# Kernel optimization log

Measured on AMD Instinct MI355X. Metric: run time of the kernel, lower is better.

The kernel has to match this reference:

```python
import jax, jax.numpy as jnp
import numpy as np

N = 50000        # nodes
E = 800000       # edges (avg degree 16)
IN = 256         # in_size
H = 4            # heads
C = 32           # out_size per head
NEG_SLOPE = 0.2  # PyG GATConv leaky_relu slope
LN_EPS = 1e-5


def setup_inputs() -> dict:
    key = jax.random.key(0)
    ks = jax.random.split(key, 6)
    x = jax.random.normal(ks[0], (N, IN), dtype=jnp.float32)
    edge_index = jax.random.randint(ks[1], (2, E), 0, N, dtype=jnp.int32)
    W = jax.random.normal(ks[2], (IN, H * C), dtype=jnp.float32) * 0.05
    att_src = jax.random.normal(ks[3], (H, C), dtype=jnp.float32) * 0.05
    att_dst = jax.random.normal(ks[4], (H, C), dtype=jnp.float32) * 0.05
    bias = jnp.zeros((H * C,), dtype=jnp.float32)
    ln_gamma = jnp.ones((H * C,), dtype=jnp.float32)
    ln_beta = jnp.zeros((H * C,), dtype=jnp.float32)
    return {"x": x, "edge_index": edge_index, "W": W, "att_src": att_src,
            "att_dst": att_dst, "bias": bias, "ln_gamma": ln_gamma,
            "ln_beta": ln_beta}


def _segment_softmax(alpha, seg, num_segments):
    # alpha: [E, H], softmax over edges sharing the same destination node.
    amax = jax.ops.segment_max(alpha, seg, num_segments=num_segments)  # [N, H]
    amax = jnp.where(jnp.isfinite(amax), amax, 0.0)  # nodes with no in-edges
    ex = jnp.exp(alpha - amax[seg])
    denom = jax.ops.segment_sum(ex, seg, num_segments=num_segments)    # [N, H]
    return ex / (denom[seg] + 1e-16)


def reference(x, edge_index, W, att_src, att_dst, bias, ln_gamma, ln_beta):
    # --- GATConv (concat=True) ---
    x_lin = (x @ W).reshape(N, H, C)                    # [N, H, C]
    a_src = jnp.sum(x_lin * att_src, axis=-1)           # [N, H]
    a_dst = jnp.sum(x_lin * att_dst, axis=-1)           # [N, H]
    src, dst = edge_index[0], edge_index[1]             # messages src -> dst
    alpha = a_src[src] + a_dst[dst]                     # [E, H]
    alpha = jnp.where(alpha >= 0, alpha, NEG_SLOPE * alpha)
    alpha = _segment_softmax(alpha, dst, N)             # [E, H]
    msg = x_lin[src] * alpha[..., None]                 # [E, H, C]
    out = jax.ops.segment_sum(msg, dst, num_segments=N) # [N, H, C]
    out = out.reshape(N, H * C) + bias                  # [N, H*C]
    # --- LayerNorm over feature dim ---
    mu = jnp.mean(out, axis=-1, keepdims=True)
    var = jnp.mean(jnp.square(out - mu), axis=-1, keepdims=True)
    out = (out - mu) * jax.lax.rsqrt(var + LN_EPS) * ln_gamma + ln_beta
    # --- activation ---
    return jax.nn.relu(out)
```

## Files before the change

### kernel.cpp

```cpp
#include <hip/hip_runtime.h>

#define NNODES 50000
#define NEDGES 800000
#define INFEAT 256
#define HC 128
#define NH 4
#define CPH 32
#define LSTRIDE 264
#define WSTR 68

typedef unsigned int uint32;
typedef unsigned short u16;
typedef short short8 __attribute__((ext_vector_type(8)));
typedef float f32x4 __attribute__((ext_vector_type(4)));

__device__ __forceinline__ float b2f(u16 s) {
    uint32 u = ((uint32)s) << 16;
    return __builtin_bit_cast(float, u);
}
__device__ __forceinline__ u16 f2bf(float x) {
    uint32 u = __builtin_bit_cast(uint32, x);
    uint32 r = (u + 0x7FFFu + ((u >> 16) & 1u)) >> 16;
    return (u16)r;
}
__device__ __forceinline__ bool probe_bf16(const void* gamma) {
    return ((const uint32*)gamma)[0] == 0x3F803F80u;
}
__device__ __forceinline__ float expleaky(float a) {
    return __expf(fmaxf(a, 0.2f * a));
}

__global__ __launch_bounds__(256) void wtp_kernel(const void* __restrict__ W,
                                                  const void* __restrict__ gm,
                                                  u16* __restrict__ wtp,
                                                  int* __restrict__ count) {
    const bool isbf = probe_bf16(gm);
    int c = blockIdx.x * 256 + threadIdx.x;
    int kt = c >> 9, nt = (c >> 6) & 7, l = c & 63;
    int r = l & 15, quad = l >> 4;
    int n = nt * 16 + r;
    int kbase = kt * 32 + quad * 8;
    u16 vals[8];
#pragma unroll
    for (int j = 0; j < 8; ++j) {
        int k = kbase + j;
        vals[j] = isbf ? ((const u16*)W)[k * HC + n] : f2bf(((const float*)W)[k * HC + n]);
    }
    *(uint4*)(wtp + (size_t)c * 8) = *(const uint4*)vals;
    uint4 z = {0u, 0u, 0u, 0u};
    uint4* cz = (uint4*)count;
    for (int i = c; i < NNODES / 4; i += 4096) cz[i] = z;
}

__global__ __launch_bounds__(256) void hist_kernel(const int* __restrict__ ei,
                                                   int* __restrict__ count,
                                                   int* __restrict__ rank) {
    int eb = blockIdx.x * 1024 + threadIdx.x;
#pragma unroll
    for (int rep = 0; rep < 4; ++rep) {
        int e = eb + rep * 256;
        if (e < NEDGES) rank[e] = atomicAdd(&count[ei[NEDGES + e]], 1);
    }
}

__global__ __launch_bounds__(256) void gemm_mfma(const void* __restrict__ x,
                                                 const uint4* __restrict__ wtp,
                                                 const void* __restrict__ att_src,
                                                 const void* __restrict__ att_dst,
                                                 const void* __restrict__ gm,
                                                 u16* __restrict__ xlin,
                                                 float* __restrict__ asrc,
                                                 float* __restrict__ adst) {
    __shared__ u16 atile[4 * 16 * LSTRIDE];
    const bool isbf = probe_bf16(gm);
    const int tid = threadIdx.x;
    const int wv = tid >> 6;
    const int lane = tid & 63;
    int wave = blockIdx.x * 4 + wv;
    int r = lane & 15;
    int quad = lane >> 4;
    int m0 = wave * 16;
    u16* my = atile + wv * (16 * LSTRIDE);

    if (isbf) {
#pragma unroll
        for (int rep = 0; rep < 8; ++rep) {
            int idx = rep * 64 + lane;
            int row = idx >> 5;
            int ch  = idx & 31;
            int gr = m0 + row;
            if (gr > NNODES - 1) gr = NNODES - 1;
            uint4 q = *(const uint4*)((const u16*)x + (size_t)gr * INFEAT + ch * 8);
            *(uint4*)(my + row * LSTRIDE + ch * 8) = q;
        }
    } else {
#pragma unroll
        for (int rep = 0; rep < 16; ++rep) {
            int idx = rep * 64 + lane;
            int row = idx >> 6;
            int c4  = idx & 63;
            int gr = m0 + row;
            if (gr > NNODES - 1) gr = NNODES - 1;
            float4 f = *(const float4*)((const float*)x + (size_t)gr * INFEAT + c4 * 4);
            u16 v[4] = {f2bf(f.x), f2bf(f.y), f2bf(f.z), f2bf(f.w)};
            *(uint2*)(my + row * LSTRIDE + c4 * 4) = *(const uint2*)v;
        }
    }

    f32x4 acc[8];
#pragma unroll
    for (int nt = 0; nt < 8; ++nt) acc[nt] = (f32x4){0.f, 0.f, 0.f, 0.f};

#pragma unroll
    for (int kt = 0; kt < 8; ++kt) {
        short8 afrag = __builtin_bit_cast(short8,
            *(const uint4*)(my + r * LSTRIDE + kt * 32 + quad * 8));
#pragma unroll
        for (int nt = 0; nt < 8; ++nt) {
            short8 bfrag = __builtin_bit_cast(short8, wtp[(kt * 8 + nt) * 64 + lane]);
            acc[nt] = __builtin_amdgcn_mfma_f32_16x16x32_bf16(afrag, bfrag, acc[nt], 0, 0, 0);
        }
    }
#pragma unroll
    for (int nt = 0; nt < 8; ++nt) {
#pragma unroll
        for (int reg = 0; reg < 4; ++reg) {
            int grow = m0 + quad * 4 + reg;
            if (grow < NNODES) xlin[(size_t)grow * HC + nt * 16 + r] = f2bf(acc[nt][reg]);
        }
    }

    float asv[8], adv[8];
#pragma unroll
    for (int nt = 0; nt < 8; ++nt) {
        int c = nt * 16 + r;
        if (isbf) {
            asv[nt] = b2f(((const u16*)att_src)[c]);
            adv[nt] = b2f(((const u16*)att_dst)[c]);
        } else {
            asv[nt] = ((const float*)att_src)[c];
            adv[nt] = ((const float*)att_dst)[c];
        }
    }
    float psrc[4][4], pdst[4][4];
#pragma unroll
    for (int h = 0; h < 4; ++h)
#pragma unroll
        for (int reg = 0; reg < 4; ++reg) { psrc[h][reg] = 0.f; pdst[h][reg] = 0.f; }
#pragma unroll
    for (int nt = 0; nt < 8; ++nt) {
        const int h = nt >> 1;
#pragma unroll
        for (int reg = 0; reg < 4; ++reg) {
            psrc[h][reg] = fmaf(acc[nt][reg], asv[nt], psrc[h][reg]);
            pdst[h][reg] = fmaf(acc[nt][reg], adv[nt], pdst[h][reg]);
        }
    }
#pragma unroll
    for (int m = 1; m < 16; m <<= 1) {
#pragma unroll
        for (int h = 0; h < 4; ++h)
#pragma unroll
            for (int reg = 0; reg < 4; ++reg) {
                psrc[h][reg] += __shfl_xor(psrc[h][reg], m);
                pdst[h][reg] += __shfl_xor(pdst[h][reg], m);
            }
    }
#pragma unroll
    for (int reg = 0; reg < 4; ++reg)
#pragma unroll
        for (int h = 0; h < 4; ++h)
            if (r == reg * 4 + h) {
                int grow = m0 + quad * 4 + reg;
                if (grow < NNODES) {
                    asrc[grow * 4 + h] = psrc[h][reg];
                    adst[grow * 4 + h] = pdst[h][reg];
                }
            }
}

__global__ __launch_bounds__(256) void blkred_kernel(const int* __restrict__ count,
                                                     int* __restrict__ blksum) {
    int i = blockIdx.x * 256 + threadIdx.x;
    int v = (i < NNODES) ? count[i] : 0;
#pragma unroll
    for (int m = 1; m < 64; m <<= 1) v += __shfl_xor(v, m);
    __shared__ int s[4];
    if ((threadIdx.x & 63) == 0) s[threadIdx.x >> 6] = v;
    __syncthreads();
    if (threadIdx.x == 0) blksum[blockIdx.x] = s[0] + s[1] + s[2] + s[3];
}

__global__ __launch_bounds__(256) void scanout_kernel(const int* __restrict__ count,
                                                      const int* __restrict__ blksum,
                                                      int* __restrict__ offsets) {
    __shared__ int sb[256];
    __shared__ int sd[256];
    const int nblk = (NNODES + 255) / 256;
    int t = threadIdx.x;
    int bv = (t < nblk) ? blksum[t] : 0;
    sb[t] = bv;
    __syncthreads();
    for (int off = 1; off < 256; off <<= 1) {
        int tv = (t >= off) ? sb[t - off] : 0;
        __syncthreads();
        sb[t] += tv;
        __syncthreads();
    }
    int base = sb[blockIdx.x] - blksum[blockIdx.x];

    int i = blockIdx.x * 256 + t;
    int v = (i < NNODES) ? count[i] : 0;
    sd[t] = v;
    __syncthreads();
    for (int off = 1; off < 256; off <<= 1) {
        int tv = (t >= off) ? sd[t - off] : 0;
        __syncthreads();
        sd[t] += tv;
        __syncthreads();
    }
    if (i < NNODES) offsets[i] = base + sd[t] - v;
    if (i == 0) offsets[NNODES] = NEDGES;
}

__global__ __launch_bounds__(256) void scatter_kernel(const int* __restrict__ ei,
                                                      const int* __restrict__ offsets,
                                                      const int* __restrict__ rank,
                                                      int* __restrict__ col) {
    int e = blockIdx.x * 256 + threadIdx.x;
    if (e >= NEDGES) return;
    int d = ei[NEDGES + e];
    col[offsets[d] + rank[e]] = ei[e];
}

__global__ __launch_bounds__(256) void node_kernel(const u16* __restrict__ xlin,
                                                   const float* __restrict__ asrc,
                                                   const float* __restrict__ adst,
                                                   const int* __restrict__ offsets,
                                                   const int* __restrict__ col,
                                                   const void* __restrict__ bias,
                                                   const void* __restrict__ gamma,
                                                   const void* __restrict__ beta,
                                                   void* __restrict__ out) {
    __shared__ float wlds[4][4 * WSTR];
    __shared__ int   slds[4][64];
    const bool isbf = probe_bf16(gamma);
    const int wv = threadIdx.x >> 6;
    const int lane = threadIdx.x & 63;
    int node = blockIdx.x * 4 + wv;
    int h = lane >> 4;
    int f2 = lane * 2;
    int start = offsets[node];
    int end = offsets[node + 1];
    float4 ad4 = *(const float4*)(adst + (size_t)node * 4);

    float dsum = 0.f, acc0 = 0.f, acc1 = 0.f;
    float* wmy = wlds[wv];
    int* smy = slds[wv];

    for (int base = start; base < end; base += 64) {
        int cnt = end - base;
        if (cnt > 64) cnt = 64;
        float4 w4 = {0.f, 0.f, 0.f, 0.f};
        int src = 0;
        if (lane < cnt) {
            src = col[base + lane];
            float4 as4 = *(const float4*)(asrc + (size_t)src * 4);
            w4.x = expleaky(as4.x + ad4.x);
            w4.y = expleaky(as4.y + ad4.y);
            w4.z = expleaky(as4.z + ad4.z);
            w4.w = expleaky(as4.w + ad4.w);
        }
        smy[lane] = src;
        wmy[0 * WSTR + lane] = w4.x;
        wmy[1 * WSTR + lane] = w4.y;
        wmy[2 * WSTR + lane] = w4.z;
        wmy[3 * WSTR + lane] = w4.w;

        const float* wh = wmy + h * WSTR;
        int j = 0;
        for (; j + 7 < cnt; j += 8) {
            float4 wa = *(const float4*)(wh + j);
            float4 wb = *(const float4*)(wh + j + 4);
            int4 sa = *(const int4*)(smy + j);
            int4 sb = *(const int4*)(smy + j + 4);
            uint32 pf[8];
            pf[0] = *(const uint32*)(xlin + (size_t)sa.x * HC + f2);
            pf[1] = *(const uint32*)(xlin + (size_t)sa.y * HC + f2);
            pf[2] = *(const uint32*)(xlin + (size_t)sa.z * HC + f2);
            pf[3] = *(const uint32*)(xlin + (size_t)sa.w * HC + f2);
            pf[4] = *(const uint32*)(xlin + (size_t)sb.x * HC + f2);
            pf[5] = *(const uint32*)(xlin + (size_t)sb.y * HC + f2);
            pf[6] = *(const uint32*)(xlin + (size_t)sb.z * HC + f2);
            pf[7] = *(const uint32*)(xlin + (size_t)sb.w * HC + f2);
            float wv8[8] = {wa.x, wa.y, wa.z, wa.w, wb.x, wb.y, wb.z, wb.w};
#pragma unroll
            for (int k = 0; k < 8; ++k) {
                float w = wv8[k];
                dsum += w;
                float x0 = __builtin_bit_cast(float, pf[k] << 16);
                float x1 = __builtin_bit_cast(float, pf[k] & 0xffff0000u);
                acc0 = fmaf(x0, w, acc0);
                acc1 = fmaf(x1, w, acc1);
            }
        }
        for (; j + 3 < cnt; j += 4) {
            float4 wa = *(const float4*)(wh + j);
            int4 sa = *(const int4*)(smy + j);
            uint32 pf[4];
            pf[0] = *(const uint32*)(xlin + (size_t)sa.x * HC + f2);
            pf[1] = *(const uint32*)(xlin + (size_t)sa.y * HC + f2);
            pf[2] = *(const uint32*)(xlin + (size_t)sa.z * HC + f2);
            pf[3] = *(const uint32*)(xlin + (size_t)sa.w * HC + f2);
            float wv4[4] = {wa.x, wa.y, wa.z, wa.w};
#pragma unroll
            for (int k = 0; k < 4; ++k) {
                float w = wv4[k];
                dsum += w;
                float x0 = __builtin_bit_cast(float, pf[k] << 16);
                float x1 = __builtin_bit_cast(float, pf[k] & 0xffff0000u);
                acc0 = fmaf(x0, w, acc0);
                acc1 = fmaf(x1, w, acc1);
            }
        }
        for (; j < cnt; ++j) {
            float w = wh[j];
            int c = smy[j];
            uint32 p = *(const uint32*)(xlin + (size_t)c * HC + f2);
            dsum += w;
            float x0 = __builtin_bit_cast(float, p << 16);
            float x1 = __builtin_bit_cast(float, p & 0xffff0000u);
            acc0 = fmaf(x0, w, acc0);
            acc1 = fmaf(x1, w, acc1);
        }
    }
    float rden = 1.f / (dsum + 1e-16f);

    float bi0, bi1, g0, g1, be0, be1;
    if (isbf) {
        uint32 bb = ((const uint32*)bias)[lane];
        uint32 gg = ((const uint32*)gamma)[lane];
        uint32 eb = ((const uint32*)beta)[lane];
        bi0 = b2f((u16)(bb & 0xffffu)); bi1 = b2f((u16)(bb >> 16));
        g0  = b2f((u16)(gg & 0xffffu)); g1  = b2f((u16)(gg >> 16));
        be0 = b2f((u16)(eb & 0xffffu)); be1 = b2f((u16)(eb >> 16));
    } else {
        float2 tb = ((const float2*)bias)[lane];
        float2 tg = ((const float2*)gamma)[lane];
        float2 te = ((const float2*)beta)[lane];
        bi0 = tb.x; bi1 = tb.y; g0 = tg.x; g1 = tg.y; be0 = te.x; be1 = te.y;
    }
    float v0 = fmaf(acc0, rden, bi0);
    float v1 = fmaf(acc1, rden, bi1);
    float s2 = v0 + v1;
    float q2 = v0 * v0 + v1 * v1;
#pragma unroll
    for (int m = 1; m < 64; m <<= 1) {
        s2 += __shfl_xor(s2, m);
        q2 += __shfl_xor(q2, m);
    }
    float mean = s2 * (1.f / 128.f);
    float var = q2 * (1.f / 128.f) - mean * mean;
    float inv = rsqrtf(var + 1e-5f);
    float d0 = v0 - mean, d1 = v1 - mean;
    float o0 = fmaxf(fmaf(d0 * inv, g0, be0), 0.f);
    float o1 = fmaxf(fmaf(d1 * inv, g1, be1), 0.f);
    if (isbf) {
        uint32 po = (uint32)f2bf(o0) | ((uint32)f2bf(o1) << 16);
        ((uint32*)out)[(size_t)node * 64 + lane] = po;
    } else {
        float2 po; po.x = o0; po.y = o1;
        ((float2*)out)[(size_t)node * 64 + lane] = po;
    }
}

extern "C" void kernel_launch(void* const* d_in, const int* in_sizes, int n_in,
                              void* d_out, int out_size, void* d_ws, size_t ws_size,
                              hipStream_t stream) {
    const void* x       = d_in[0];
    const int*  ei      = (const int*)d_in[1];
    const void* W       = d_in[2];
    const void* att_src = d_in[3];
    const void* att_dst = d_in[4];
    const void* bias    = d_in[5];
    const void* gamma   = d_in[6];
    const void* beta    = d_in[7];

    char* w = (char*)d_ws;
    size_t off = 0;
    u16* xlin    = (u16*)(w + off);   off += 12800000;
    u16* wtp     = (u16*)(w + off);   off += 65536;
    float* asrc  = (float*)(w + off); off += 800000;
    float* adst  = (float*)(w + off); off += 800000;
    int* count   = (int*)(w + off);   off += 200000;
    int* offsets = (int*)(w + off);   off += 200016;
    int* rank    = (int*)(w + off);   off += 3200000;
    int* blksum  = (int*)(w + off);   off += 1024;
    int* col     = (int*)(w + off);   off += 3200000;

    const int NBLK = (NNODES + 255) / 256;
    wtp_kernel<<<16, 256, 0, stream>>>(W, gamma, wtp, count);
    hist_kernel<<<(NEDGES + 1023) / 1024, 256, 0, stream>>>(ei, count, rank);
    gemm_mfma<<<(NNODES + 63) / 64, 256, 0, stream>>>(x, (const uint4*)wtp, att_src, att_dst,
                                                      gamma, xlin, asrc, adst);
    blkred_kernel<<<NBLK, 256, 0, stream>>>(count, blksum);
    scanout_kernel<<<NBLK, 256, 0, stream>>>(count, blksum, offsets);
    scatter_kernel<<<(NEDGES + 255) / 256, 256, 0, stream>>>(ei, offsets, rank, col);
    node_kernel<<<NNODES / 4, 256, 0, stream>>>(xlin, asrc, adst, offsets, col,
                                                bias, gamma, beta, d_out);
}
```

Baseline: 212.7 us.

## Replace global atomic degree histogram with per-block LDS histograms plus column prefix

Degree counting no longer does one global atomicAdd per edge. The edges are split across 64 blocks, and each block builds a packed 16-bit histogram in a 100KB shared-memory array and writes it to global memory. A new colsum kernel turns these per-block histograms into per-block base offsets and total counts, and the scatter kernel adds the base for the edge's block when placing it. This removes contended global atomics but launches only 64 blocks and adds about 19MB of extra global traffic plus a random base lookup per edge in scatter.

```diff
diff --git a/kernel.cpp b/kernel.cpp
--- a/kernel.cpp
+++ b/kernel.cpp
@@ -8,6 +8,8 @@
 #define CPH 32
 #define LSTRIDE 264
 #define WSTR 68
+#define NB 64
+#define EPB (NEDGES / NB)
 
 typedef unsigned int uint32;
 typedef unsigned short u16;
@@ -32,8 +34,7 @@
 
 __global__ __launch_bounds__(256) void wtp_kernel(const void* __restrict__ W,
                                                   const void* __restrict__ gm,
-                                                  u16* __restrict__ wtp,
-                                                  int* __restrict__ count) {
+                                                  u16* __restrict__ wtp) {
     const bool isbf = probe_bf16(gm);
     int c = blockIdx.x * 256 + threadIdx.x;
     int kt = c >> 9, nt = (c >> 6) & 7, l = c & 63;
@@ -47,20 +48,41 @@
         vals[j] = isbf ? ((const u16*)W)[k * HC + n] : f2bf(((const float*)W)[k * HC + n]);
     }
     *(uint4*)(wtp + (size_t)c * 8) = *(const uint4*)vals;
-    uint4 z = {0u, 0u, 0u, 0u};
-    uint4* cz = (uint4*)count;
-    for (int i = c; i < NNODES / 4; i += 4096) cz[i] = z;
-}
-
-__global__ __launch_bounds__(256) void hist_kernel(const int* __restrict__ ei,
-                                                   int* __restrict__ count,
-                                                   int* __restrict__ rank) {
-    int eb = blockIdx.x * 1024 + threadIdx.x;
-#pragma unroll
-    for (int rep = 0; rep < 4; ++rep) {
-        int e = eb + rep * 256;
-        if (e < NEDGES) rank[e] = atomicAdd(&count[ei[NEDGES + e]], 1);
-    }
+}
+
+__global__ __launch_bounds__(256) void histm_kernel(const int* __restrict__ ei,
+                                                    uint32* __restrict__ hist,
+                                                    int* __restrict__ rank) {
+    __shared__ uint32 hl[NNODES / 2];
+    const int t = threadIdx.x;
+    const int blk = blockIdx.x;
+    for (int i = t; i < NNODES / 2; i += 256) hl[i] = 0u;
+    __syncthreads();
+    const int e0 = blk * EPB;
+    for (int i = t; i < EPB; i += 256) {
+        int e = e0 + i;
+        int d = ei[NEDGES + e];
+        uint32 add = (d & 1) ? 0x10000u : 1u;
+        uint32 old = atomicAdd(&hl[d >> 1], add);
+        rank[e] = (d & 1) ? (int)(old >> 16) : (int)(old & 0xffffu);
+    }
+    __syncthreads();
+    uint32* hrow = hist + (size_t)blk * (NNODES / 2);
+    for (int i = t; i < NNODES / 2; i += 256) hrow[i] = hl[i];
+}
+
+__global__ __launch_bounds__(256) void colsum_kernel(const uint32* __restrict__ hist,
+                                                     int* __restrict__ count,
+                                                     int* __restrict__ base) {
+    int node = blockIdx.x * 256 + threadIdx.x;
+    if (node >= NNODES) return;
+    const u16* h16 = (const u16*)hist;
+    int acc = 0;
+    for (int b = 0; b < NB; ++b) {
+        base[(size_t)b * NNODES + node] = acc;
+        acc += (int)h16[(size_t)b * NNODES + node];
+    }
+    count[node] = acc;
 }
 
 __global__ __launch_bounds__(256) void gemm_mfma(const void* __restrict__ x,
@@ -225,12 +247,14 @@
 
 __global__ __launch_bounds__(256) void scatter_kernel(const int* __restrict__ ei,
                                                       const int* __restrict__ offsets,
+                                                      const int* __restrict__ base,
                                                       const int* __restrict__ rank,
                                                       int* __restrict__ col) {
     int e = blockIdx.x * 256 + threadIdx.x;
     if (e >= NEDGES) return;
     int d = ei[NEDGES + e];
-    col[offsets[d] + rank[e]] = ei[e];
+    int blk = e / EPB;
+    col[offsets[d] + base[(size_t)blk * NNODES + d] + rank[e]] = ei[e];
 }
 
 __global__ __launch_bounds__(256) void node_kernel(const u16* __restrict__ xlin,
@@ -397,15 +421,19 @@
     int* rank    = (int*)(w + off);   off += 3200000;
     int* blksum  = (int*)(w + off);   off += 1024;
     int* col     = (int*)(w + off);   off += 3200000;
+    uint32* hist = (uint32*)(w + off); off += (size_t)NB * (NNODES / 2) * 4;
+    int* baseم   = nullptr; (void)baseم;
+    int* basem   = (int*)(w + off);   off += (size_t)NB * NNODES * 4;
 
     const int NBLK = (NNODES + 255) / 256;
-    wtp_kernel<<<16, 256, 0, stream>>>(W, gamma, wtp, count);
-    hist_kernel<<<(NEDGES + 1023) / 1024, 256, 0, stream>>>(ei, count, rank);
+    wtp_kernel<<<16, 256, 0, stream>>>(W, gamma, wtp);
+    histm_kernel<<<NB, 256, 0, stream>>>(ei, hist, rank);
     gemm_mfma<<<(NNODES + 63) / 64, 256, 0, stream>>>(x, (const uint4*)wtp, att_src, att_dst,
                                                       gamma, xlin, asrc, adst);
+    colsum_kernel<<<(NNODES + 255) / 256, 256, 0, stream>>>(hist, count, basem);
     blkred_kernel<<<NBLK, 256, 0, stream>>>(count, blksum);
     scanout_kernel<<<NBLK, 256, 0, stream>>>(count, blksum, offsets);
-    scatter_kernel<<<(NEDGES + 255) / 256, 256, 0, stream>>>(ei, offsets, rank, col);
+    scatter_kernel<<<(NEDGES + 255) / 256, 256, 0, stream>>>(ei, offsets, basem, rank, col);
     node_kernel<<<NNODES / 4, 256, 0, stream>>>(xlin, asrc, adst, offsets, col,
                                                 bias, gamma, beta, d_out);
 }
```

Result: no change. 214.3 us (+0.7%).
